# Performance work log

Measured on AMD Instinct MI355X. Metric: run time of the kernel, lower is better.

Reference implementation:

```python
import jax, jax.numpy as jnp
import numpy as np

B, N = 8, 4096
NPOINT, RADIUS, NSAMPLE = 1024, 0.5, 32
IN_C = 64
MLP = [64, 64, 128]
EPS = 1e-5


def _gather(p, idx):
    # p: (B,N,C), idx: (B,...) int -> (B,...,C)
    return jax.vmap(lambda a, i: a[i])(p, idx)


def farthest_point_sample(xyz, npoint):
    b, n, _ = xyz.shape
    def step(carry, _):
        distance, farthest = carry
        centroid = _gather(xyz, farthest[:, None])              # (B,1,3)
        d = jnp.sum((xyz - centroid) ** 2, axis=-1)             # (B,N)
        distance = jnp.minimum(distance, d)
        nxt = jnp.argmax(distance, axis=-1).astype(jnp.int32)
        return (distance, nxt), farthest
    init = (jnp.full((b, n), 1e10, xyz.dtype), jnp.zeros((b,), jnp.int32))
    _, idx = jax.lax.scan(step, init, None, length=npoint)
    return idx.T                                                 # (B,npoint)


def query_ball_point(radius, nsample, xyz, new_xyz):
    b, n, _ = xyz.shape
    s = new_xyz.shape[1]
    sqr = jnp.sum((new_xyz[:, :, None, :] - xyz[:, None, :, :]) ** 2, axis=-1)  # (B,S,N)
    grp = jnp.broadcast_to(jnp.arange(n, dtype=jnp.int32), (b, s, n))
    grp = jnp.where(sqr > radius ** 2, n, grp)
    grp = jnp.sort(grp, axis=-1)[:, :, :nsample]                 # (B,S,K)
    first = grp[:, :, :1]
    return jnp.where(grp == n, first, grp)


def _sa_forward(xyz, points, params):
    fps_idx = farthest_point_sample(xyz, NPOINT)
    new_xyz = _gather(xyz, fps_idx)                              # (B,S,3)
    idx = query_ball_point(RADIUS, NSAMPLE, xyz, new_xyz)        # (B,S,K)
    grouped_xyz = _gather(xyz, idx)                              # (B,S,K,3)
    grouped_norm = grouped_xyz - new_xyz[:, :, None, :]
    grouped_pts = _gather(points, idx)                           # (B,S,K,C)
    feat = jnp.concatenate([grouped_xyz, grouped_norm, grouped_pts], axis=-1)
    for w, bias, gamma, beta in params:
        feat = jnp.einsum('bski,oi->bsko', feat, w) + bias       # 1x1 conv
        mean = feat.mean(axis=(0, 1, 2))                         # BN (train stats)
        var = feat.var(axis=(0, 1, 2))
        feat = (feat - mean) * jax.lax.rsqrt(var + EPS) * gamma + beta
        feat = jax.nn.relu(feat)
    new_points = feat.max(axis=2)                                # max over neighbors
    return new_xyz, new_points


def setup_inputs() -> dict:
    key = jax.random.key(0)
    ks = jax.random.split(key, 8)
    inp = {
        'xyz': jax.random.normal(ks[0], (B, N, 3), jnp.float32),
        'points': jax.random.normal(ks[1], (B, N, IN_C), jnp.float32),
    }
    last = IN_C + 6
    for li, out in enumerate(MLP):
        inp[f'w{li}'] = jax.random.normal(ks[2 + li], (out, last), jnp.float32) * 0.05
        inp[f'b{li}'] = jnp.zeros((out,), jnp.float32)
        inp[f'g{li}'] = jnp.ones((out,), jnp.float32)
        inp[f'be{li}'] = jnp.zeros((out,), jnp.float32)
        last = out
    return inp


def reference(xyz, points, w0, b0, g0, be0, w1, b1, g1, be1, w2, b2, g2, be2):
    params = [(w0, b0, g0, be0), (w1, b1, g1, be1), (w2, b2, g2, be2)]
    return _sa_forward(xyz, points, params)
```

## Files before the change

kernel.cpp:

```cpp
#include <hip/hip_runtime.h>

#define DI __device__ __forceinline__

#define B_ 8
#define N_ 4096
#define S_ 1024
#define K_ 32
#define M_TOT (B_ * S_ * K_)
#define NBLK 2048
#define NW 4096

typedef short bf16x8 __attribute__((ext_vector_type(8)));
typedef float f32x4 __attribute__((ext_vector_type(4)));

DI float sqdist_rn(float ax, float ay, float az, float bx, float by, float bz) {
    float dx = __fsub_rn(ax, bx);
    float dy = __fsub_rn(ay, by);
    float dz = __fsub_rn(az, bz);
    return __fadd_rn(__fadd_rn(__fmul_rn(dx, dx), __fmul_rn(dy, dy)), __fmul_rn(dz, dz));
}

DI unsigned short f2b(float f) {
    unsigned u = __float_as_uint(f);
    return (unsigned short)((u + 0x7FFFu + ((u >> 16) & 1u)) >> 16);
}
DI float b2f(unsigned short h) { return __uint_as_float(((unsigned)h) << 16); }

template <int CTRL>
DI unsigned long long dpp_u64(unsigned long long v) {
    unsigned lo = (unsigned)__builtin_amdgcn_update_dpp(
        0, (int)(unsigned)v, CTRL, 0xF, 0xF, true);
    unsigned hi = (unsigned)__builtin_amdgcn_update_dpp(
        0, (int)(unsigned)(v >> 32), CTRL, 0xF, 0xF, true);
    return ((unsigned long long)hi << 32) | lo;
}
DI unsigned long long umax64(unsigned long long a, unsigned long long b) {
    return a > b ? a : b;
}

struct FpsSh { float4 pts[N_]; unsigned long long part[2][8]; };
struct WrkSh { float feat[128 * 76]; float wl[64 * 76]; int idxl[128]; };
union MegaSh { FpsSh f; WrkSh w; char pad[84 * 1024]; };

DI void fps_role(const float* __restrict__ xyz, float* __restrict__ new_xyz,
                 unsigned* __restrict__ cnt, MegaSh& sh) {
    const int b = blockIdx.x;
    const int t = threadIdx.x;
    const float* X = xyz + (size_t)b * (N_ * 3);
    float px[8], py[8], pz[8], dd[8];
#pragma unroll
    for (int j = 0; j < 8; ++j) {
        int p = t + 512 * j;
        float x = X[p * 3 + 0], y = X[p * 3 + 1], z = X[p * 3 + 2];
        px[j] = x; py[j] = y; pz[j] = z; dd[j] = 1e10f;
        sh.f.pts[p] = make_float4(x, y, z, 0.0f);
    }
    if (t == 0) {
        new_xyz[(size_t)b * (S_ * 3) + 0] = px[0];
        new_xyz[(size_t)b * (S_ * 3) + 1] = py[0];
        new_xyz[(size_t)b * (S_ * 3) + 2] = pz[0];
    }
    __syncthreads();
    float4 cent = sh.f.pts[0];
    for (int i = 1; i < S_; ++i) {
        unsigned long long k0[8];
#pragma unroll
        for (int j = 0; j < 8; ++j) {
            float d = sqdist_rn(px[j], py[j], pz[j], cent.x, cent.y, cent.z);
            dd[j] = fminf(dd[j], d);
            k0[j] = ((unsigned long long)__float_as_uint(dd[j]) << 32) |
                    (unsigned long long)(~(unsigned)(t + 512 * j));
        }
        k0[0] = umax64(k0[0], k0[1]);
        k0[2] = umax64(k0[2], k0[3]);
        k0[4] = umax64(k0[4], k0[5]);
        k0[6] = umax64(k0[6], k0[7]);
        k0[0] = umax64(k0[0], k0[2]);
        k0[4] = umax64(k0[4], k0[6]);
        unsigned long long key = umax64(k0[0], k0[4]);
        key = umax64(key, dpp_u64<0x111>(key));
        key = umax64(key, dpp_u64<0x112>(key));
        key = umax64(key, dpp_u64<0x114>(key));
        key = umax64(key, dpp_u64<0x118>(key));
        key = umax64(key, dpp_u64<0x142>(key));
        key = umax64(key, dpp_u64<0x143>(key));
        if ((t & 63) == 63) sh.f.part[i & 1][t >> 6] = key;
        __syncthreads();
        ulonglong2 q0 = *(const ulonglong2*)&sh.f.part[i & 1][0];
        ulonglong2 q1 = *(const ulonglong2*)&sh.f.part[i & 1][2];
        ulonglong2 q2 = *(const ulonglong2*)&sh.f.part[i & 1][4];
        ulonglong2 q3 = *(const ulonglong2*)&sh.f.part[i & 1][6];
        unsigned long long ka = umax64(umax64(q0.x, q0.y), umax64(q1.x, q1.y));
        unsigned long long kb = umax64(umax64(q2.x, q2.y), umax64(q3.x, q3.y));
        unsigned long long k = umax64(ka, kb);
        unsigned gidx = ~(unsigned)(k & 0xFFFFFFFFull);
        cent = sh.f.pts[gidx];
        if (t == 0) {
            size_t o3 = ((size_t)b * S_ + i) * 3;
            new_xyz[o3 + 0] = cent.x;
            new_xyz[o3 + 1] = cent.y;
            new_xyz[o3 + 2] = cent.z;
            if ((i & 31) == 31) {
                __threadfence();
                __hip_atomic_store(&cnt[b], (unsigned)(i + 1),
                                   __ATOMIC_RELEASE, __HIP_MEMORY_SCOPE_AGENT);
            }
        }
    }
}

DI void gemm512(const float* __restrict__ feat, const float* __restrict__ wl,
                const float* __restrict__ bias, unsigned short* __restrict__ yout,
                float* __restrict__ ps, float* __restrict__ pq, int tile, int tid) {
    const int tr = tid & 15;
    const int tc = tid >> 4;
    const int r0 = tile * 128;
    float acc[8][2];
#pragma unroll
    for (int rr = 0; rr < 8; ++rr) { acc[rr][0] = 0.f; acc[rr][1] = 0.f; }
#pragma unroll 2
    for (int sl = 0; sl < 18; ++sl) {
        float4 xv[8], wv[2];
#pragma unroll
        for (int rr = 0; rr < 8; ++rr)
            xv[rr] = *(const float4*)&feat[(tr + 16 * rr) * 76 + 4 * sl];
#pragma unroll
        for (int cc = 0; cc < 2; ++cc)
            wv[cc] = *(const float4*)&wl[(tc + 32 * cc) * 76 + 4 * sl];
#pragma unroll
        for (int rr = 0; rr < 8; ++rr)
#pragma unroll
            for (int cc = 0; cc < 2; ++cc)
                acc[rr][cc] = fmaf(xv[rr].x, wv[cc].x,
                               fmaf(xv[rr].y, wv[cc].y,
                                fmaf(xv[rr].z, wv[cc].z,
                                 fmaf(xv[rr].w, wv[cc].w, acc[rr][cc]))));
    }
#pragma unroll
    for (int cc = 0; cc < 2; ++cc) {
        const int och = tc + 32 * cc;
        const float bv = bias[och];
        float s1 = 0.f, s2 = 0.f;
#pragma unroll
        for (int rr = 0; rr < 8; ++rr) {
            float y = acc[rr][cc] + bv;
            yout[(size_t)(r0 + tr + 16 * rr) * 64 + och] = f2b(y);
            s1 += y;
            s2 = fmaf(y, y, s2);
        }
#pragma unroll
        for (int m = 1; m < 16; m <<= 1) {
            s1 += __shfl_xor(s1, m);
            s2 += __shfl_xor(s2, m);
        }
        if ((tid & 15) == 0) {
            ps[och * NBLK + tile] = s1;
            pq[och * NBLK + tile] = s2;
        }
    }
}

DI void worker_role(const float* __restrict__ xyz, const float* __restrict__ points,
                    const float* __restrict__ new_xyz, const float* __restrict__ W0,
                    const float* __restrict__ bias0, unsigned short* __restrict__ yout,
                    float* __restrict__ ps, float* __restrict__ pq,
                    const unsigned* __restrict__ cnt, MegaSh& sh, int nWrk) {
    const int t = threadIdx.x;
    for (int g = (int)blockIdx.x - 8; g < 2048; g += nWrk) {
        const int q = g >> 3;
        const int b = g & 7;
        const int s0 = q * 4;
        const int tile = b * 256 + q;
        if (t == 0) {
            while (__hip_atomic_load(&cnt[b], __ATOMIC_ACQUIRE,
                                     __HIP_MEMORY_SCOPE_AGENT) < (unsigned)(s0 + 4))
                __builtin_amdgcn_s_sleep(32);
        }
        __syncthreads();
        const int w = t >> 6, lane = t & 63;
        if (w < 4) {
            const int c = b * 1024 + s0 + w;
            const float* X = xyz + (size_t)b * (N_ * 3);
            const float cx = new_xyz[c * 3 + 0];
            const float cy = new_xyz[c * 3 + 1];
            const float cz = new_xyz[c * 3 + 2];
            int* out = &sh.w.idxl[w * K_];
            int taken = 0, first = -1;
            for (int ch = 0; ch < 64; ++ch) {
                int p = ch * 64 + lane;
                float d = sqdist_rn(X[p * 3 + 0], X[p * 3 + 1], X[p * 3 + 2], cx, cy, cz);
                bool ok = (d <= 0.25f);
                unsigned long long m = __ballot(ok);
                if (first < 0 && m) first = ch * 64 + (__ffsll((unsigned long long)m) - 1);
                int pos = taken + (int)__popcll(m & ((1ull << lane) - 1ull));
                if (ok && pos < K_) out[pos] = p;
                taken += (int)__popcll(m);
                if (taken >= K_) break;
            }
            int filled = taken < K_ ? taken : K_;
            if (lane >= filled && lane < K_) out[lane] = first;
        }
        __syncthreads();
        for (int jj = t; jj < 64 * 70; jj += 512) {
            int o = jj / 70;
            int i2 = jj - o * 70;
            int mch = (i2 < 6) ? i2 : (i2 + 2);
            sh.w.wl[o * 76 + mch] = W0[jj];
        }
        if (t < 128) sh.w.wl[(t >> 1) * 76 + 6 + (t & 1)] = 0.0f;
        {
            const int row = t >> 2, h = t & 3;
            const int k = row & 31, cloc = row >> 5;
            const int pi = sh.w.idxl[cloc * 32 + k];
            const float* P = points + ((size_t)b * N_ + pi) * 64 + h * 16;
            float* fr = &sh.w.feat[row * 76];
#pragma unroll
            for (int qq = 0; qq < 4; ++qq)
                *(float4*)(fr + 8 + h * 16 + 4 * qq) = *(const float4*)(P + 4 * qq);
            if (h == 0) {
                size_t pb = ((size_t)b * N_ + pi) * 3;
                float x = xyz[pb + 0], y = xyz[pb + 1], z = xyz[pb + 2];
                const float* C = new_xyz + ((size_t)b * S_ + s0 + cloc) * 3;
                fr[0] = x; fr[1] = y; fr[2] = z;
                fr[3] = x - C[0]; fr[4] = y - C[1]; fr[5] = z - C[2];
                fr[6] = 0.0f; fr[7] = 0.0f;
            }
        }
        __syncthreads();
        gemm512(sh.w.feat, sh.w.wl, bias0, yout, ps, pq, tile, t);
        __syncthreads();
    }
}

__global__ __launch_bounds__(512) void mega_kernel(
    const float* __restrict__ xyz, const float* __restrict__ points,
    float* __restrict__ new_xyz, const float* __restrict__ w0,
    const float* __restrict__ b0, unsigned short* __restrict__ y1,
    float* __restrict__ ps, float* __restrict__ pq,
    unsigned* __restrict__ cnt, int nWrk) {
    __shared__ MegaSh sh;
    if (blockIdx.x < 8)
        fps_role(xyz, new_xyz, cnt, sh);
    else
        worker_role(xyz, points, new_xyz, w0, b0, y1, ps, pq, cnt, sh, nWrk);
}

template <int OC, bool LAST>
__global__ __launch_bounds__(256) void layerM_kernel(
    const unsigned short* __restrict__ yin,
    const float* __restrict__ scale, const float* __restrict__ shift,
    const float* __restrict__ W, const float* __restrict__ bias,
    unsigned short* __restrict__ yout,
    float* __restrict__ ps, float* __restrict__ pq,
    float* __restrict__ maxb, float* __restrict__ minb) {
    const int tid = threadIdx.x;
    const int blk = blockIdx.x;
    const int r0 = blk * 256;
    __shared__ unsigned short featA[256 * 64];
    __shared__ unsigned short wlT[OC * 64];
    __shared__ float ssc[64], ssh[64];
    if (tid < 64) { ssc[tid] = scale[tid]; ssh[tid] = shift[tid]; }
#pragma unroll
    for (int it = 0; it < OC / 16; ++it) {
        int q = it * 256 + tid;
        int och = q >> 4;
        int qq = q & 15;
        float4 wv = *(const float4*)&W[q * 4];
        uint2 pk;
        pk.x = (unsigned)f2b(wv.x) | ((unsigned)f2b(wv.y) << 16);
        pk.y = (unsigned)f2b(wv.z) | ((unsigned)f2b(wv.w) << 16);
        int idx = och * 64 + (((qq * 8) ^ ((och & 7) << 4)) >> 1);
        *(uint2*)&wlT[idx] = pk;
    }
    __syncthreads();
#pragma unroll
    for (int it = 0; it < 8; ++it) {
        int f = it * 256 + tid;
        int row = f >> 3, g = f & 7;
        uint4 u = *(const uint4*)&yin[(size_t)(r0 + row) * 64 + g * 8];
        int c = g * 8;
        float f0 = fmaxf(fmaf(__uint_as_float(u.x << 16),         ssc[c + 0], ssh[c + 0]), 0.f);
        float f1 = fmaxf(fmaf(__uint_as_float(u.x & 0xFFFF0000u), ssc[c + 1], ssh[c + 1]), 0.f);
        float f2 = fmaxf(fmaf(__uint_as_float(u.y << 16),         ssc[c + 2], ssh[c + 2]), 0.f);
        float f3 = fmaxf(fmaf(__uint_as_float(u.y & 0xFFFF0000u), ssc[c + 3], ssh[c + 3]), 0.f);
        float f4 = fmaxf(fmaf(__uint_as_float(u.z << 16),         ssc[c + 4], ssh[c + 4]), 0.f);
        float f5 = fmaxf(fmaf(__uint_as_float(u.z & 0xFFFF0000u), ssc[c + 5], ssh[c + 5]), 0.f);
        float f6 = fmaxf(fmaf(__uint_as_float(u.w << 16),         ssc[c + 6], ssh[c + 6]), 0.f);
        float f7 = fmaxf(fmaf(__uint_as_float(u.w & 0xFFFF0000u), ssc[c + 7], ssh[c + 7]), 0.f);
        uint4 pk;
        pk.x = (unsigned)f2b(f0) | ((unsigned)f2b(f1) << 16);
        pk.y = (unsigned)f2b(f2) | ((unsigned)f2b(f3) << 16);
        pk.z = (unsigned)f2b(f4) | ((unsigned)f2b(f5) << 16);
        pk.w = (unsigned)f2b(f6) | ((unsigned)f2b(f7) << 16);
        int idx = row * 64 + (((g * 16) ^ ((row & 7) << 4)) >> 1);
        *(uint4*)&featA[idx] = pk;
    }
    __syncthreads();
    const int w = tid >> 6, l = tid & 63;
    const int lr = l & 15, lg = l >> 4;
    const int wrow0 = w * 64;
    f32x4 acc[4][OC / 16];
#pragma unroll
    for (int mf = 0; mf < 4; ++mf)
#pragma unroll
        for (int nf = 0; nf < OC / 16; ++nf)
#pragma unroll
            for (int r = 0; r < 4; ++r) acc[mf][nf][r] = 0.0f;
#pragma unroll
    for (int kc = 0; kc < 2; ++kc) {
        const int kb = kc * 64 + lg * 16;
        bf16x8 bfr[OC / 16];
#pragma unroll
        for (int nf = 0; nf < OC / 16; ++nf) {
            int och = nf * 16 + lr;
            bfr[nf] = *(const bf16x8*)&wlT[och * 64 + ((kb ^ ((och & 7) << 4)) >> 1)];
        }
#pragma unroll
        for (int mf = 0; mf < 4; ++mf) {
            int row = wrow0 + mf * 16 + lr;
            bf16x8 af = *(const bf16x8*)&featA[row * 64 + ((kb ^ ((row & 7) << 4)) >> 1)];
#pragma unroll
            for (int nf = 0; nf < OC / 16; ++nf)
                acc[mf][nf] = __builtin_amdgcn_mfma_f32_16x16x32_bf16(
                    af, bfr[nf], acc[mf][nf], 0, 0, 0);
        }
    }
    const int gwave = blk * 4 + w;
#pragma unroll
    for (int nf = 0; nf < OC / 16; ++nf) {
        const int och = nf * 16 + lr;
        const float bv = bias[och];
        float s1 = 0.f, s2 = 0.f;
        float mx0 = -1e30f, mn0 = 1e30f, mx1 = -1e30f, mn1 = 1e30f;
#pragma unroll
    for (int mf = 0; mf < 4; ++mf) {
#pragma unroll
            for (int r = 0; r < 4; ++r) {
                float y = acc[mf][nf][r] + bv;
                s1 += y;
                s2 = fmaf(y, y, s2);
                if (LAST) {
                    if (mf < 2) { mx0 = fmaxf(mx0, y); mn0 = fminf(mn0, y); }
                    else        { mx1 = fmaxf(mx1, y); mn1 = fminf(mn1, y); }
                } else {
                    int gr = r0 + wrow0 + mf * 16 + lg * 4 + r;
                    yout[(size_t)gr * OC + och] = f2b(y);
                }
            }
        }
        s1 += __shfl_xor(s1, 16); s1 += __shfl_xor(s1, 32);
        s2 += __shfl_xor(s2, 16); s2 += __shfl_xor(s2, 32);
        if (LAST) {
            mx0 = fmaxf(mx0, __shfl_xor(mx0, 16)); mx0 = fmaxf(mx0, __shfl_xor(mx0, 32));
            mn0 = fminf(mn0, __shfl_xor(mn0, 16)); mn0 = fminf(mn0, __shfl_xor(mn0, 32));
            mx1 = fmaxf(mx1, __shfl_xor(mx1, 16)); mx1 = fmaxf(mx1, __shfl_xor(mx1, 32));
            mn1 = fminf(mn1, __shfl_xor(mn1, 16)); mn1 = fminf(mn1, __shfl_xor(mn1, 32));
        }
        if (l < 16) {
            ps[och * NW + gwave] = s1;
            pq[och * NW + gwave] = s2;
            if (LAST) {
                int grp0 = blk * 8 + w * 2;
                maxb[(size_t)grp0 * OC + och] = mx0;
                minb[(size_t)grp0 * OC + och] = mn0;
                maxb[(size_t)(grp0 + 1) * OC + och] = mx1;
                minb[(size_t)(grp0 + 1) * OC + och] = mn1;
            }
        }
    }
}

template <int NPART>
__global__ __launch_bounds__(256) void bn_reduce_kernel(
    const float* __restrict__ ps, const float* __restrict__ pq,
    const float* __restrict__ gamma, const float* __restrict__ beta,
    float* __restrict__ scale, float* __restrict__ shift) {
    const int o = blockIdx.x, t = threadIdx.x;
    float s1 = 0.f, s2 = 0.f;
    for (int i = t; i < NPART; i += 256) {
        s1 += ps[o * NPART + i];
        s2 += pq[o * NPART + i];
    }
#pragma unroll
    for (int m = 32; m >= 1; m >>= 1) { s1 += __shfl_xor(s1, m); s2 += __shfl_xor(s2, m); }
    __shared__ float a1[4], a2[4];
    if ((t & 63) == 0) { a1[t >> 6] = s1; a2[t >> 6] = s2; }
    __syncthreads();
    if (t == 0) {
        float S1 = a1[0] + a1[1] + a1[2] + a1[3];
        float S2 = a2[0] + a2[1] + a2[2] + a2[3];
        const float inv = 1.0f / (float)M_TOT;
        float mean = S1 * inv;
        float var = S2 * inv - mean * mean;
        if (var < 0.f) var = 0.f;
        float rstd = 1.0f / sqrtf(var + 1e-5f);
        float sc = rstd * gamma[o];
        scale[o] = sc;
        shift[o] = beta[o] - mean * sc;
    }
}

__global__ __launch_bounds__(256) void pool2_kernel(
    const float* __restrict__ maxb, const float* __restrict__ minb,
    const float* __restrict__ scale, const float* __restrict__ shift,
    float* __restrict__ outp) {
    int idx = blockIdx.x * 256 + threadIdx.x;
    int och = idx & 127;
    float sc = scale[och], sh = shift[och];
    float a = fmaf(maxb[idx], sc, sh);
    float b = fmaf(minb[idx], sc, sh);
    outp[idx] = fmaxf(fmaxf(a, b), 0.0f);
}

extern "C" void kernel_launch(void* const* d_in, const int* in_sizes, int n_in,
                              void* d_out, int out_size, void* d_ws, size_t ws_size,
                              hipStream_t stream) {
    const float* xyz    = (const float*)d_in[0];
    const float* points = (const float*)d_in[1];
    const float* w0  = (const float*)d_in[2];
    const float* b0  = (const float*)d_in[3];
    const float* g0  = (const float*)d_in[4];
    const float* be0 = (const float*)d_in[5];
    const float* w1  = (const float*)d_in[6];
    const float* b1  = (const float*)d_in[7];
    const float* g1  = (const float*)d_in[8];
    const float* be1 = (const float*)d_in[9];
    const float* w2  = (const float*)d_in[10];
    const float* b2  = (const float*)d_in[11];
    const float* g2  = (const float*)d_in[12];
    const float* be2 = (const float*)d_in[13];

    float* out = (float*)d_out;
    char* ws = (char*)d_ws;
    unsigned* cnt = (unsigned*)ws;
    float* ps  = (float*)(ws + (1 << 20));
    float* pq  = (float*)(ws + (3 << 20));
    float* st  = (float*)(ws + (5 << 20));
    float *sc0 = st,        *sh0 = st + 128;
    float *sc1 = st + 256,  *sh1 = st + 384;
    float *sc2 = st + 512,  *sh2 = st + 640;
    float* maxb = (float*)(ws + (6 << 20));
    float* minb = (float*)(ws + (10 << 20));
    unsigned short* y1 = (unsigned short*)(ws + (14 << 20));
    unsigned short* y2 = (unsigned short*)(ws + (46 << 20));

    int blocksPerCU = 0;
    hipOccupancyMaxActiveBlocksPerMultiprocessor(&blocksPerCU, mega_kernel, 512, 0);
    if (blocksPerCU < 1) blocksPerCU = 1;
    int grid = blocksPerCU * 256;
    if (grid > 2056) grid = 2056;
    int nWrk = grid - 8;

    hipMemsetAsync(cnt, 0, 8 * sizeof(unsigned), stream);

    void* args[] = {(void*)&xyz, (void*)&points, (void*)&out, (void*)&w0, (void*)&b0,
                    (void*)&y1, (void*)&ps, (void*)&pq, (void*)&cnt, (void*)&nWrk};
    hipLaunchCooperativeKernel(mega_kernel, dim3(grid), dim3(512), args, 0, stream);

    bn_reduce_kernel<NBLK><<<64, 256, 0, stream>>>(ps, pq, g0, be0, sc0, sh0);
    layerM_kernel<64, false><<<M_TOT / 256, 256, 0, stream>>>(
        y1, sc0, sh0, w1, b1, y2, ps, pq, nullptr, nullptr);
    bn_reduce_kernel<NW><<<64, 256, 0, stream>>>(ps, pq, g1, be1, sc1, sh1);
    layerM_kernel<128, true><<<M_TOT / 256, 256, 0, stream>>>(
        y2, sc1, sh1, w2, b2, nullptr, ps, pq, maxb, minb);
    bn_reduce_kernel<NW><<<128, 256, 0, stream>>>(ps, pq, g2, be2, sc2, sh2);
    pool2_kernel<<<4096, 256, 0, stream>>>(maxb, minb, sc2, sh2, out + 24576);
}
```

Baseline: 856.5 us.

## Batch FPS centroid publication and pad progress counters to separate cache lines

The FPS role now records selected indices in shared memory and writes new_xyz coordinates in batches of 32 from 32 threads, instead of having thread 0 issue a global store every iteration. The release store of the progress counter is deferred to the next iteration, after the barrier, so the threadfence and atomic leave the serial critical path. Per-batch counters are padded to separate cache lines to avoid false sharing between spinning workers, and the worker spin sleep is lengthened. This targets the serial FPS loop latency, at the cost of more shared memory and slightly delayed publication to workers.

```diff
diff --git a/kernel.cpp b/kernel.cpp
--- a/kernel.cpp
+++ b/kernel.cpp
@@ -9,6 +9,7 @@
 #define M_TOT (B_ * S_ * K_)
 #define NBLK 2048
 #define NW 4096
+#define CSTRIDE 32
 
 typedef short bf16x8 __attribute__((ext_vector_type(8)));
 typedef float f32x4 __attribute__((ext_vector_type(4)));
@@ -38,7 +39,11 @@
     return a > b ? a : b;
 }
 
-struct FpsSh { float4 pts[N_]; unsigned long long part[2][8]; };
+struct FpsSh {
+    float4 pts[N_];
+    unsigned long long part[2][8];
+    unsigned idxs[S_];
+};
 struct WrkSh { float feat[128 * 76]; float wl[64 * 76]; int idxl[128]; };
 union MegaSh { FpsSh f; WrkSh w; char pad[84 * 1024]; };
 
@@ -55,13 +60,11 @@
         px[j] = x; py[j] = y; pz[j] = z; dd[j] = 1e10f;
         sh.f.pts[p] = make_float4(x, y, z, 0.0f);
     }
-    if (t == 0) {
-        new_xyz[(size_t)b * (S_ * 3) + 0] = px[0];
-        new_xyz[(size_t)b * (S_ * 3) + 1] = py[0];
-        new_xyz[(size_t)b * (S_ * 3) + 2] = pz[0];
-    }
+    if (t == 0) sh.f.idxs[0] = 0;
     __syncthreads();
     float4 cent = sh.f.pts[0];
+    unsigned pubbase = 0;
+    unsigned relval = 0;
     for (int i = 1; i < S_; ++i) {
         unsigned long long k0[8];
 #pragma unroll
@@ -86,6 +89,12 @@
         key = umax64(key, dpp_u64<0x143>(key));
         if ((t & 63) == 63) sh.f.part[i & 1][t >> 6] = key;
         __syncthreads();
+        if (relval != 0) {
+            if (t == 0)
+                __hip_atomic_store(&cnt[b * CSTRIDE], relval,
+                                   __ATOMIC_RELEASE, __HIP_MEMORY_SCOPE_AGENT);
+            relval = 0;
+        }
         ulonglong2 q0 = *(const ulonglong2*)&sh.f.part[i & 1][0];
         ulonglong2 q1 = *(const ulonglong2*)&sh.f.part[i & 1][2];
         ulonglong2 q2 = *(const ulonglong2*)&sh.f.part[i & 1][4];
@@ -95,18 +104,37 @@
         unsigned long long k = umax64(ka, kb);
         unsigned gidx = ~(unsigned)(k & 0xFFFFFFFFull);
         cent = sh.f.pts[gidx];
-        if (t == 0) {
-            size_t o3 = ((size_t)b * S_ + i) * 3;
-            new_xyz[o3 + 0] = cent.x;
-            new_xyz[o3 + 1] = cent.y;
-            new_xyz[o3 + 2] = cent.z;
-            if ((i & 31) == 31) {
+        if (t == 0) sh.f.idxs[i] = gidx;
+        if (pubbase + 32 <= (unsigned)i) {
+            if (t < 32) {
+                unsigned j = pubbase + (unsigned)t;
+                float4 p = sh.f.pts[sh.f.idxs[j]];
+                size_t o3 = ((size_t)b * S_ + j) * 3;
+                new_xyz[o3 + 0] = p.x;
+                new_xyz[o3 + 1] = p.y;
+                new_xyz[o3 + 2] = p.z;
                 __threadfence();
-                __hip_atomic_store(&cnt[b], (unsigned)(i + 1),
-                                   __ATOMIC_RELEASE, __HIP_MEMORY_SCOPE_AGENT);
             }
-        }
-    }
+            relval = pubbase + 32;
+            pubbase += 32;
+        }
+    }
+    __syncthreads();
+    if (relval != 0 && t == 0)
+        __hip_atomic_store(&cnt[b * CSTRIDE], relval,
+                           __ATOMIC_RELEASE, __HIP_MEMORY_SCOPE_AGENT);
+    for (unsigned j = pubbase + (unsigned)t; j < S_; j += 512) {
+        float4 p = sh.f.pts[sh.f.idxs[j]];
+        size_t o3 = ((size_t)b * S_ + j) * 3;
+        new_xyz[o3 + 0] = p.x;
+        new_xyz[o3 + 1] = p.y;
+        new_xyz[o3 + 2] = p.z;
+    }
+    __threadfence();
+    __syncthreads();
+    if (t == 0)
+        __hip_atomic_store(&cnt[b * CSTRIDE], (unsigned)S_,
+                           __ATOMIC_RELEASE, __HIP_MEMORY_SCOPE_AGENT);
 }
 
 DI void gemm512(const float* __restrict__ feat, const float* __restrict__ wl,
@@ -172,9 +200,9 @@
         const int s0 = q * 4;
         const int tile = b * 256 + q;
         if (t == 0) {
-            while (__hip_atomic_load(&cnt[b], __ATOMIC_ACQUIRE,
+            while (__hip_atomic_load(&cnt[b * CSTRIDE], __ATOMIC_ACQUIRE,
                                      __HIP_MEMORY_SCOPE_AGENT) < (unsigned)(s0 + 4))
-                __builtin_amdgcn_s_sleep(32);
+                __builtin_amdgcn_s_sleep(64);
         }
         __syncthreads();
         const int w = t >> 6, lane = t & 63;
@@ -451,7 +479,7 @@
     if (grid > 2056) grid = 2056;
     int nWrk = grid - 8;
 
-    hipMemsetAsync(cnt, 0, 8 * sizeof(unsigned), stream);
+    hipMemsetAsync(cnt, 0, 8 * CSTRIDE * sizeof(unsigned), stream);
 
     void* args[] = {(void*)&xyz, (void*)&points, (void*)&out, (void*)&w0, (void*)&b0,
                     (void*)&y1, (void*)&ps, (void*)&pq, (void*)&cnt, (void*)&nWrk};
```

Result: slower. 876.1 us (+2.3%).
